# Kernel tuning notes

Measured on AMD Instinct MI355X. Metric: run time of the kernel, lower is better.

Reference implementation:

```python
import jax, jax.numpy as jnp
import numpy as np

TOP_K = 2


def setup_inputs() -> dict:
    key = jax.random.key(0)
    k0, k1, k2, k3 = jax.random.split(key, 4)
    B, S, H, I, E = 4, 2048, 1024, 2048, 8
    x = jax.random.normal(k0, (B, S, H), dtype=jnp.float32)
    Wr = jax.random.normal(k1, (H, E), dtype=jnp.float32) * 0.02
    W1 = jax.random.normal(k2, (E, H, 2 * I), dtype=jnp.float32) * 0.02
    W2 = jax.random.normal(k3, (E, I, H), dtype=jnp.float32) * 0.02
    return {"x": x, "Wr": Wr, "W1": W1, "W2": W2}


def reference(x, Wr, W1, W2):
    B, S, H = x.shape
    E = W1.shape[0]
    I = W2.shape[1]
    xf = x.reshape(-1, H)  # [T, H], T = B*S

    # Top-k router
    logits = xf @ Wr                              # [T, E]
    probs = jax.nn.softmax(logits, axis=-1)
    rw, sel = jax.lax.top_k(probs, TOP_K)          # [T, k], [T, k]
    rw = rw.astype(jnp.float32)
    rw = rw / rw.sum(axis=-1, keepdims=True)

    out = jnp.zeros_like(xf)
    for e in range(E):
        # combined gate weight for this expert per token (0 if not routed here)
        g = (rw * (sel == e)).sum(axis=-1)         # [T]
        h = xf @ W1[e]                             # [T, 2I]
        gate, up = h[:, :I], h[:, I:]
        eo = (jax.nn.silu(gate) * up) @ W2[e]      # [T, H]
        out = out + g[:, None] * eo
    return out.reshape(B, S, H)
```

## Files before the change

### kernel.cpp

```cpp
#include <hip/hip_runtime.h>
#include <hip/hip_bf16.h>

#define NTOK   8192
#define HDIM   1024
#define NEXP   8
#define IDIM   2048
#define TOTAL  (NTOK*2)

typedef short bf16x8 __attribute__((ext_vector_type(8)));
typedef float f32x4  __attribute__((ext_vector_type(4)));

__device__ __forceinline__ unsigned short f2bf(float f) {
  __hip_bfloat16 h = __float2bfloat16(f);
  return *reinterpret_cast<unsigned short*>(&h);
}
__device__ __forceinline__ float bf2f(unsigned short u) {
  __hip_bfloat16 h = *reinterpret_cast<__hip_bfloat16*>(&u);
  return __bfloat162float(h);
}

__device__ __forceinline__ void lds_load16(const unsigned short* gsrc, unsigned short* lds_base_uniform) {
  __builtin_amdgcn_global_load_lds(
      (const __attribute__((address_space(1))) unsigned int*)gsrc,
      (__attribute__((address_space(3))) unsigned int*)lds_base_uniform,
      16, 0, 0);
}

__global__ void router_kernel(const float* __restrict__ x, const float* __restrict__ Wr,
                              int* __restrict__ sel, float* __restrict__ selw,
                              int* __restrict__ counts) {
  int t = blockIdx.x * 4 + (threadIdx.x >> 6);
  int lane = threadIdx.x & 63;
  float acc[NEXP];
#pragma unroll
  for (int e = 0; e < NEXP; ++e) acc[e] = 0.f;
  const float* xr = x + (size_t)t * HDIM;
  for (int h = lane; h < HDIM; h += 64) {
    float xv = xr[h];
    const float* wr = Wr + h * NEXP;
#pragma unroll
    for (int e = 0; e < NEXP; ++e) acc[e] += xv * wr[e];
  }
#pragma unroll
  for (int off = 32; off > 0; off >>= 1) {
#pragma unroll
    for (int e = 0; e < NEXP; ++e) acc[e] += __shfl_xor(acc[e], off, 64);
  }
  if (lane == 0) {
    int i0 = 0; float v0 = acc[0];
#pragma unroll
    for (int e = 1; e < NEXP; ++e) if (acc[e] > v0) { v0 = acc[e]; i0 = e; }
    int i1 = -1; float v1 = -1e30f;
#pragma unroll
    for (int e = 0; e < NEXP; ++e) if (e != i0 && acc[e] > v1) { v1 = acc[e]; i1 = e; }
    float e1 = expf(v1 - v0);
    float w0 = 1.f / (1.f + e1);
    float w1 = e1 / (1.f + e1);
    sel[t*2] = i0; sel[t*2+1] = i1;
    selw[t*2] = w0; selw[t*2+1] = w1;
    atomicAdd(&counts[i0], 1);
    atomicAdd(&counts[i1], 1);
  }
}

__global__ void prefix_kernel(const int* __restrict__ counts, int* __restrict__ offsets,
                              int* __restrict__ cursor) {
  if (threadIdx.x == 0) {
    int s = 0;
    for (int e = 0; e < NEXP; ++e) { offsets[e] = s; cursor[e] = s; s += counts[e]; }
    offsets[NEXP] = s;
  }
}

__global__ void scatter_kernel(const int* __restrict__ sel, const float* __restrict__ selw,
                               int* __restrict__ cursor, int* __restrict__ token_ids,
                               float* __restrict__ gates) {
  int t = blockIdx.x * 256 + threadIdx.x;
  if (t >= NTOK) return;
#pragma unroll
  for (int k = 0; k < 2; ++k) {
    int e = sel[t*2+k];
    int p = atomicAdd(&cursor[e], 1);
    token_ids[p] = t;
    gates[p] = selw[t*2+k];
  }
}

__global__ void xsplit_kernel(const float* __restrict__ x, unsigned short* __restrict__ Xs) {
  int t = blockIdx.x;
  const float4* src = reinterpret_cast<const float4*>(x + (size_t)t * HDIM);
  float4 v = src[threadIdx.x];
  unsigned short h0 = f2bf(v.x), h1 = f2bf(v.y), h2 = f2bf(v.z), h3 = f2bf(v.w);
  ushort4 hi = { h0, h1, h2, h3 };
  ushort4 lo = { f2bf(v.x - bf2f(h0)), f2bf(v.y - bf2f(h1)),
                 f2bf(v.z - bf2f(h2)), f2bf(v.w - bf2f(h3)) };
  *reinterpret_cast<ushort4*>(Xs + (size_t)t*2*HDIM + threadIdx.x*4) = hi;
  *reinterpret_cast<ushort4*>(Xs + (size_t)t*2*HDIM + HDIM + threadIdx.x*4) = lo;
}

__global__ void split_transpose_kernel(const float* __restrict__ W, unsigned short* __restrict__ WT,
                                       int R, int C) {
  int e = blockIdx.z;
  int c0 = blockIdx.x * 64, r0 = blockIdx.y * 64;
  __shared__ unsigned short hiT[64][65];
  __shared__ unsigned short loT[64][65];
  int tx = threadIdx.x & 63, ty = threadIdx.x >> 6;
  const float* src = W + ((size_t)e * R + r0) * C + c0;
#pragma unroll
  for (int rr = 0; rr < 16; ++rr) {
    int r_l = ty * 16 + rr;
    float v = src[(size_t)r_l * C + tx];
    unsigned short h = f2bf(v);
    hiT[tx][r_l] = h;
    loT[tx][r_l] = f2bf(v - bf2f(h));
  }
  __syncthreads();
  unsigned short* dst = WT + ((size_t)e * C + c0) * (size_t)(2*R) + r0;
#pragma unroll
  for (int ww = 0; ww < 16; ++ww) {
    int c_l = ty * 16 + ww;
    dst[(size_t)c_l * (2*R) + tx]     = hiT[c_l][tx];
    dst[(size_t)c_l * (2*R) + R + tx] = loT[c_l][tx];
  }
}

__global__ __launch_bounds__(256)
void gemm1_kernel(const unsigned short* __restrict__ Xs,
                  const unsigned short* __restrict__ W1sT,
                  unsigned short* __restrict__ actS,
                  const int* __restrict__ offsets,
                  const int* __restrict__ token_ids) {
  int e = blockIdx.z;
  int off = offsets[e];
  int cnt = offsets[e+1] - off;
  int r0 = blockIdx.x * 128;
  if (r0 >= cnt) return;
  int j0 = blockIdx.y * 64;

  __shared__ unsigned short As[128*32];
  __shared__ unsigned short Bg[64*32];
  __shared__ unsigned short Bu[64*32];

  int tid = threadIdx.x;
  int lane = tid & 63, wv = tid >> 6;
  int l15 = lane & 15, lq = lane >> 4;

  f32x4 accg[2][4], accu[2][4];
#pragma unroll
  for (int m = 0; m < 2; ++m)
#pragma unroll
    for (int n = 0; n < 4; ++n) {
      accg[m][n] = f32x4{0.f, 0.f, 0.f, 0.f};
      accu[m][n] = f32x4{0.f, 0.f, 0.f, 0.f};
    }

  const unsigned short* w1e = W1sT + (size_t)e * 4096 * 2048;

  int oa0 = wv*1024 + lane*16;
  int oa1 = 4096 + oa0;
  int rowA0 = oa0 >> 6, cbA0 = (oa0 & 63) >> 1;
  int rowA1 = oa1 >> 6, cbA1 = (oa1 & 63) >> 1;
  int gpA0 = off + r0 + rowA0; if (gpA0 > TOTAL-1) gpA0 = TOTAL-1;
  int gpA1 = off + r0 + rowA1; if (gpA1 > TOTAL-1) gpA1 = TOTAL-1;
  int tA0 = token_ids[gpA0];
  int tA1 = token_ids[gpA1];
  const unsigned short* srcA0 = Xs + (size_t)tA0*2048 + cbA0;
  const unsigned short* srcA1 = Xs + (size_t)tA1*2048 + cbA1;
  int ob = wv*1024 + lane*16;
  int colB = ob >> 6, kbB = (ob & 63) >> 1;

  for (int ks = 0; ks < 96; ++ks) {
    int s  = ks >> 5;
    int k0 = (ks & 31) << 5;
    int acol = ((s == 1) ? HDIM : 0) + k0;
    int bk   = ((s == 2) ? HDIM : 0) + k0;

    lds_load16(srcA0 + acol, (unsigned short*)((char*)As + wv*1024));
    lds_load16(srcA1 + acol, (unsigned short*)((char*)As + 4096 + wv*1024));
    lds_load16(w1e + (size_t)(j0 + colB)*2048 + bk + kbB,        (unsigned short*)((char*)Bg + wv*1024));
    lds_load16(w1e + (size_t)(IDIM + j0 + colB)*2048 + bk + kbB, (unsigned short*)((char*)Bu + wv*1024));
    __syncthreads();

    bf16x8 af[2], bgf[4], buf2[4];
#pragma unroll
    for (int m = 0; m < 2; ++m)
      af[m] = *reinterpret_cast<const bf16x8*>(&As[(wv*32 + m*16 + l15)*32 + lq*8]);
#pragma unroll
    for (int n = 0; n < 4; ++n) {
      bgf[n]  = *reinterpret_cast<const bf16x8*>(&Bg[(n*16 + l15)*32 + lq*8]);
      buf2[n] = *reinterpret_cast<const bf16x8*>(&Bu[(n*16 + l15)*32 + lq*8]);
    }
#pragma unroll
    for (int m = 0; m < 2; ++m)
#pragma unroll
      for (int n = 0; n < 4; ++n) {
        accg[m][n] = __builtin_amdgcn_mfma_f32_16x16x32_bf16(af[m], bgf[n], accg[m][n], 0, 0, 0);
        accu[m][n] = __builtin_amdgcn_mfma_f32_16x16x32_bf16(af[m], buf2[n], accu[m][n], 0, 0, 0);
      }
    __syncthreads();
  }

#pragma unroll
  for (int m = 0; m < 2; ++m) {
#pragma unroll
    for (int rr = 0; rr < 4; ++rr) {
      int lrow = r0 + wv*32 + m*16 + lq*4 + rr;
      if (lrow < cnt) {
        size_t prow = (size_t)(off + lrow);
#pragma unroll
        for (int n = 0; n < 4; ++n) {
          float g = accg[m][n][rr], u = accu[m][n][rr];
          float a = (g / (1.f + expf(-g))) * u;
          unsigned short hh = f2bf(a);
          unsigned short ll = f2bf(a - bf2f(hh));
          int col = j0 + n*16 + l15;
          actS[prow*4096 + col]        = hh;
          actS[prow*4096 + IDIM + col] = ll;
        }
      }
    }
  }
}

__global__ __launch_bounds__(256)
void gemm2_kernel(const unsigned short* __restrict__ actS,
                  const unsigned short* __restrict__ W2sT,
                  const int* __restrict__ offsets,
                  const int* __restrict__ token_ids,
                  const float* __restrict__ gates,
                  float* __restrict__ out) {
  int e = blockIdx.z;
  int off = offsets[e];
  int cnt = offsets[e+1] - off;
  int r0 = blockIdx.x * 128;
  if (r0 >= cnt) return;
  int c0 = blockIdx.y * 128;

  __shared__ unsigned short As[128*32];
  __shared__ unsigned short Bs[128*32];

  int tid = threadIdx.x;
  int lane = tid & 63, wv = tid >> 6;
  int l15 = lane & 15, lq = lane >> 4;

  f32x4 acc[2][8];
#pragma unroll
  for (int m = 0; m < 2; ++m)
#pragma unroll
    for (int n = 0; n < 8; ++n) acc[m][n] = f32x4{0.f, 0.f, 0.f, 0.f};

  const unsigned short* w2e = W2sT + (size_t)e * 1024 * 4096;

  int oa0 = wv*1024 + lane*16;
  int oa1 = 4096 + oa0;
  int rowA0 = oa0 >> 6, cbA0 = (oa0 & 63) >> 1;
  int rowA1 = oa1 >> 6, cbA1 = (oa1 & 63) >> 1;
  int gpA0 = off + r0 + rowA0; if (gpA0 > TOTAL-1) gpA0 = TOTAL-1;
  int gpA1 = off + r0 + rowA1; if (gpA1 > TOTAL-1) gpA1 = TOTAL-1;
  int colB0 = oa0 >> 6, kbB0 = (oa0 & 63) >> 1;
  int colB1 = oa1 >> 6, kbB1 = (oa1 & 63) >> 1;

  for (int ks = 0; ks < 192; ++ks) {
    int s  = ks >> 6;
    int k0 = (ks & 63) << 5;
    int acol = ((s == 1) ? IDIM : 0) + k0;
    int bk   = ((s == 2) ? IDIM : 0) + k0;

    lds_load16(actS + (size_t)gpA0*4096 + acol + cbA0, (unsigned short*)((char*)As + wv*1024));
    lds_load16(actS + (size_t)gpA1*4096 + acol + cbA1, (unsigned short*)((char*)As + 4096 + wv*1024));
    lds_load16(w2e + (size_t)(c0 + colB0)*4096 + bk + kbB0, (unsigned short*)((char*)Bs + wv*1024));
    lds_load16(w2e + (size_t)(c0 + colB1)*4096 + bk + kbB1, (unsigned short*)((char*)Bs + 4096 + wv*1024));
    __syncthreads();

    bf16x8 af[2], bfr[8];
#pragma unroll
    for (int m = 0; m < 2; ++m)
      af[m] = *reinterpret_cast<const bf16x8*>(&As[(wv*32 + m*16 + l15)*32 + lq*8]);
#pragma unroll
    for (int n = 0; n < 8; ++n)
      bfr[n] = *reinterpret_cast<const bf16x8*>(&Bs[(n*16 + l15)*32 + lq*8]);
#pragma unroll
    for (int m = 0; m < 2; ++m)
#pragma unroll
      for (int n = 0; n < 8; ++n)
        acc[m][n] = __builtin_amdgcn_mfma_f32_16x16x32_bf16(af[m], bfr[n], acc[m][n], 0, 0, 0);
    __syncthreads();
  }

#pragma unroll
  for (int m = 0; m < 2; ++m) {
#pragma unroll
    for (int rr = 0; rr < 4; ++rr) {
      int lrow = r0 + wv*32 + m*16 + lq*4 + rr;
      if (lrow < cnt) {
        int pos = off + lrow;
        int t = token_ids[pos];
        float w = gates[pos];
        float* orow = out + (size_t)t * HDIM;
#pragma unroll
        for (int n = 0; n < 8; ++n)
          atomicAdd(&orow[c0 + n*16 + l15], w * acc[m][n][rr]);
      }
    }
  }
}

extern "C" void kernel_launch(void* const* d_in, const int* in_sizes, int n_in,
                              void* d_out, int out_size, void* d_ws, size_t ws_size,
                              hipStream_t stream) {
  (void)in_sizes; (void)n_in;
  const float* x  = (const float*)d_in[0];
  const float* Wr = (const float*)d_in[1];
  const float* W1 = (const float*)d_in[2];
  const float* W2 = (const float*)d_in[3];
  float* out = (float*)d_out;

  char* ws = (char*)d_ws;
  int*   counts    = (int*)(ws + 0);
  int*   offsets   = (int*)(ws + 64);
  int*   cursor    = (int*)(ws + 128);
  int*   sel       = (int*)(ws + 4096);
  float* selw      = (float*)(ws + 4096 + 65536);
  int*   token_ids = (int*)(ws + 4096 + 2*65536);
  float* gates     = (float*)(ws + 4096 + 3*65536);
  const size_t XS_OFF   = 266240ULL;
  const size_t W1T_OFF  = XS_OFF  + 33554432ULL;
  const size_t W2T_OFF  = W1T_OFF + 134217728ULL;
  const size_t ACT_OFF  = W2T_OFF + 67108864ULL;
  const size_t REQUIRED = ACT_OFF + 134217728ULL;
  unsigned short* Xs   = (unsigned short*)(ws + XS_OFF);
  unsigned short* W1sT = (unsigned short*)(ws + W1T_OFF);
  unsigned short* W2sT = (unsigned short*)(ws + W2T_OFF);
  unsigned short* actS = (unsigned short*)(ws + ACT_OFF);

  hipMemsetAsync(d_out, 0, (size_t)out_size * sizeof(float), stream);
  if (ws_size < REQUIRED) return;

  hipMemsetAsync(counts, 0, 64, stream);
  router_kernel<<<NTOK/4, 256, 0, stream>>>(x, Wr, sel, selw, counts);
  prefix_kernel<<<1, 64, 0, stream>>>(counts, offsets, cursor);
  scatter_kernel<<<NTOK/256, 256, 0, stream>>>(sel, selw, cursor, token_ids, gates);
  xsplit_kernel<<<NTOK, 256, 0, stream>>>(x, Xs);
  split_transpose_kernel<<<dim3(64, 16, NEXP), 256, 0, stream>>>(W1, W1sT, 1024, 4096);
  split_transpose_kernel<<<dim3(16, 32, NEXP), 256, 0, stream>>>(W2, W2sT, 2048, 1024);
  gemm1_kernel<<<dim3(64, 32, NEXP), 256, 0, stream>>>(Xs, W1sT, actS, offsets, token_ids);
  gemm2_kernel<<<dim3(64, 8, NEXP), 256, 0, stream>>>(actS, W2sT, offsets, token_ids, gates, out);
}
```

Before: 1.986 ms.

## Double K tile to 64 with XOR-swizzled LDS layout in both MoE GEMMs

```diff
diff --git a/kernel.cpp b/kernel.cpp
--- a/kernel.cpp
+++ b/kernel.cpp
@@ -137,13 +137,39 @@
   if (r0 >= cnt) return;
   int j0 = blockIdx.y * 64;
 
-  __shared__ unsigned short As[128*32];
-  __shared__ unsigned short Bg[64*32];
-  __shared__ unsigned short Bu[64*32];
+  __shared__ unsigned short As[128*64];
+  __shared__ unsigned short Bg[64*64];
+  __shared__ unsigned short Bu[64*64];
 
   int tid = threadIdx.x;
   int lane = tid & 63, wv = tid >> 6;
   int l15 = lane & 15, lq = lane >> 4;
+  int lr = lane >> 3;
+  int g  = lane & 7;
+
+  const unsigned short* w1e = W1sT + (size_t)e * 4096 * 2048;
+
+  const unsigned short* srcA[4]; unsigned short* dstA[4];
+#pragma unroll
+  for (int i = 0; i < 4; ++i) {
+    int rowt = wv*32 + i*8 + lr;
+    int gp = off + r0 + rowt; if (gp > TOTAL-1) gp = TOTAL-1;
+    int tok = token_ids[gp];
+    int sg = g ^ (rowt & 7);
+    srcA[i] = Xs + (size_t)tok*2048 + sg*8;
+    dstA[i] = As + wv*2048 + i*512;
+  }
+  const unsigned short* srcBg[2]; const unsigned short* srcBu[2];
+  unsigned short* dstBg[2]; unsigned short* dstBu[2];
+#pragma unroll
+  for (int i = 0; i < 2; ++i) {
+    int rowt = wv*16 + i*8 + lr;
+    int sg = g ^ (rowt & 7);
+    srcBg[i] = w1e + (size_t)(j0 + rowt)*2048 + sg*8;
+    srcBu[i] = w1e + (size_t)(IDIM + j0 + rowt)*2048 + sg*8;
+    dstBg[i] = Bg + wv*1024 + i*512;
+    dstBu[i] = Bu + wv*1024 + i*512;
+  }
 
   f32x4 accg[2][4], accu[2][4];
 #pragma unroll
@@ -154,49 +180,41 @@
       accu[m][n] = f32x4{0.f, 0.f, 0.f, 0.f};
     }
 
-  const unsigned short* w1e = W1sT + (size_t)e * 4096 * 2048;
-
-  int oa0 = wv*1024 + lane*16;
-  int oa1 = 4096 + oa0;
-  int rowA0 = oa0 >> 6, cbA0 = (oa0 & 63) >> 1;
-  int rowA1 = oa1 >> 6, cbA1 = (oa1 & 63) >> 1;
-  int gpA0 = off + r0 + rowA0; if (gpA0 > TOTAL-1) gpA0 = TOTAL-1;
-  int gpA1 = off + r0 + rowA1; if (gpA1 > TOTAL-1) gpA1 = TOTAL-1;
-  int tA0 = token_ids[gpA0];
-  int tA1 = token_ids[gpA1];
-  const unsigned short* srcA0 = Xs + (size_t)tA0*2048 + cbA0;
-  const unsigned short* srcA1 = Xs + (size_t)tA1*2048 + cbA1;
-  int ob = wv*1024 + lane*16;
-  int colB = ob >> 6, kbB = (ob & 63) >> 1;
-
-  for (int ks = 0; ks < 96; ++ks) {
-    int s  = ks >> 5;
-    int k0 = (ks & 31) << 5;
-    int acol = ((s == 1) ? HDIM : 0) + k0;
-    int bk   = ((s == 2) ? HDIM : 0) + k0;
-
-    lds_load16(srcA0 + acol, (unsigned short*)((char*)As + wv*1024));
-    lds_load16(srcA1 + acol, (unsigned short*)((char*)As + 4096 + wv*1024));
-    lds_load16(w1e + (size_t)(j0 + colB)*2048 + bk + kbB,        (unsigned short*)((char*)Bg + wv*1024));
-    lds_load16(w1e + (size_t)(IDIM + j0 + colB)*2048 + bk + kbB, (unsigned short*)((char*)Bu + wv*1024));
+  for (int ks = 0; ks < 48; ++ks) {
+    int s  = ks >> 4;
+    int k0 = (ks & 15) << 6;
+    int aoff = ((s == 1) ? HDIM : 0) + k0;
+    int boff = ((s == 2) ? HDIM : 0) + k0;
+
+#pragma unroll
+    for (int i = 0; i < 4; ++i) lds_load16(srcA[i] + aoff, dstA[i]);
+#pragma unroll
+    for (int i = 0; i < 2; ++i) {
+      lds_load16(srcBg[i] + boff, dstBg[i]);
+      lds_load16(srcBu[i] + boff, dstBu[i]);
+    }
     __syncthreads();
 
-    bf16x8 af[2], bgf[4], buf2[4];
-#pragma unroll
-    for (int m = 0; m < 2; ++m)
-      af[m] = *reinterpret_cast<const bf16x8*>(&As[(wv*32 + m*16 + l15)*32 + lq*8]);
-#pragma unroll
-    for (int n = 0; n < 4; ++n) {
-      bgf[n]  = *reinterpret_cast<const bf16x8*>(&Bg[(n*16 + l15)*32 + lq*8]);
-      buf2[n] = *reinterpret_cast<const bf16x8*>(&Bu[(n*16 + l15)*32 + lq*8]);
-    }
-#pragma unroll
-    for (int m = 0; m < 2; ++m)
+#pragma unroll
+    for (int kk = 0; kk < 2; ++kk) {
+      int gg = ((kk*4 + lq) ^ (l15 & 7)) * 8;
+      bf16x8 af[2], bgf[4], buf2[4];
+#pragma unroll
+      for (int m = 0; m < 2; ++m)
+        af[m] = *reinterpret_cast<const bf16x8*>(&As[(wv*32 + m*16 + l15)*64 + gg]);
 #pragma unroll
       for (int n = 0; n < 4; ++n) {
-        accg[m][n] = __builtin_amdgcn_mfma_f32_16x16x32_bf16(af[m], bgf[n], accg[m][n], 0, 0, 0);
-        accu[m][n] = __builtin_amdgcn_mfma_f32_16x16x32_bf16(af[m], buf2[n], accu[m][n], 0, 0, 0);
+        bgf[n]  = *reinterpret_cast<const bf16x8*>(&Bg[(n*16 + l15)*64 + gg]);
+        buf2[n] = *reinterpret_cast<const bf16x8*>(&Bu[(n*16 + l15)*64 + gg]);
       }
+#pragma unroll
+      for (int m = 0; m < 2; ++m)
+#pragma unroll
+        for (int n = 0; n < 4; ++n) {
+          accg[m][n] = __builtin_amdgcn_mfma_f32_16x16x32_bf16(af[m], bgf[n], accg[m][n], 0, 0, 0);
+          accu[m][n] = __builtin_amdgcn_mfma_f32_16x16x32_bf16(af[m], buf2[n], accu[m][n], 0, 0, 0);
+        }
+    }
     __syncthreads();
   }
 
@@ -209,8 +227,8 @@
         size_t prow = (size_t)(off + lrow);
 #pragma unroll
         for (int n = 0; n < 4; ++n) {
-          float g = accg[m][n][rr], u = accu[m][n][rr];
-          float a = (g / (1.f + expf(-g))) * u;
+          float gte = accg[m][n][rr], u = accu[m][n][rr];
+          float a = (gte / (1.f + expf(-gte))) * u;
           unsigned short hh = f2bf(a);
           unsigned short ll = f2bf(a - bf2f(hh));
           int col = j0 + n*16 + l15;
@@ -236,12 +254,29 @@
   if (r0 >= cnt) return;
   int c0 = blockIdx.y * 128;
 
-  __shared__ unsigned short As[128*32];
-  __shared__ unsigned short Bs[128*32];
+  __shared__ unsigned short As[128*64];
+  __shared__ unsigned short Bs[128*64];
 
   int tid = threadIdx.x;
   int lane = tid & 63, wv = tid >> 6;
   int l15 = lane & 15, lq = lane >> 4;
+  int lr = lane >> 3;
+  int g  = lane & 7;
+
+  const unsigned short* w2e = W2sT + (size_t)e * 1024 * 4096;
+
+  const unsigned short* srcA[4]; unsigned short* dstA[4];
+  const unsigned short* srcB[4]; unsigned short* dstB[4];
+#pragma unroll
+  for (int i = 0; i < 4; ++i) {
+    int rowt = wv*32 + i*8 + lr;
+    int gp = off + r0 + rowt; if (gp > TOTAL-1) gp = TOTAL-1;
+    int sg = g ^ (rowt & 7);
+    srcA[i] = actS + (size_t)gp*4096 + sg*8;
+    dstA[i] = As + wv*2048 + i*512;
+    srcB[i] = w2e + (size_t)(c0 + rowt)*4096 + sg*8;
+    dstB[i] = Bs + wv*2048 + i*512;
+  }
 
   f32x4 acc[2][8];
 #pragma unroll
@@ -249,41 +284,35 @@
 #pragma unroll
     for (int n = 0; n < 8; ++n) acc[m][n] = f32x4{0.f, 0.f, 0.f, 0.f};
 
-  const unsigned short* w2e = W2sT + (size_t)e * 1024 * 4096;
-
-  int oa0 = wv*1024 + lane*16;
-  int oa1 = 4096 + oa0;
-  int rowA0 = oa0 >> 6, cbA0 = (oa0 & 63) >> 1;
-  int rowA1 = oa1 >> 6, cbA1 = (oa1 & 63) >> 1;
-  int gpA0 = off + r0 + rowA0; if (gpA0 > TOTAL-1) gpA0 = TOTAL-1;
-  int gpA1 = off + r0 + rowA1; if (gpA1 > TOTAL-1) gpA1 = TOTAL-1;
-  int colB0 = oa0 >> 6, kbB0 = (oa0 & 63) >> 1;
-  int colB1 = oa1 >> 6, kbB1 = (oa1 & 63) >> 1;
-
-  for (int ks = 0; ks < 192; ++ks) {
-    int s  = ks >> 6;
-    int k0 = (ks & 63) << 5;
-    int acol = ((s == 1) ? IDIM : 0) + k0;
-    int bk   = ((s == 2) ? IDIM : 0) + k0;
-
-    lds_load16(actS + (size_t)gpA0*4096 + acol + cbA0, (unsigned short*)((char*)As + wv*1024));
-    lds_load16(actS + (size_t)gpA1*4096 + acol + cbA1, (unsigned short*)((char*)As + 4096 + wv*1024));
-    lds_load16(w2e + (size_t)(c0 + colB0)*4096 + bk + kbB0, (unsigned short*)((char*)Bs + wv*1024));
-    lds_load16(w2e + (size_t)(c0 + colB1)*4096 + bk + kbB1, (unsigned short*)((char*)Bs + 4096 + wv*1024));
+  for (int ks = 0; ks < 96; ++ks) {
+    int s  = ks >> 5;
+    int k0 = (ks & 31) << 6;
+    int aoff = ((s == 1) ? IDIM : 0) + k0;
+    int boff = ((s == 2) ? IDIM : 0) + k0;
+
+#pragma unroll
+    for (int i = 0; i < 4; ++i) {
+      lds_load16(srcA[i] + aoff, dstA[i]);
+      lds_load16(srcB[i] + boff, dstB[i]);
+    }
     __syncthreads();
 
-    bf16x8 af[2], bfr[8];
-#pragma unroll
-    for (int m = 0; m < 2; ++m)
-      af[m] = *reinterpret_cast<const bf16x8*>(&As[(wv*32 + m*16 + l15)*32 + lq*8]);
-#pragma unroll
-    for (int n = 0; n < 8; ++n)
-      bfr[n] = *reinterpret_cast<const bf16x8*>(&Bs[(n*16 + l15)*32 + lq*8]);
-#pragma unroll
-    for (int m = 0; m < 2; ++m)
+#pragma unroll
+    for (int kk = 0; kk < 2; ++kk) {
+      int gg = ((kk*4 + lq) ^ (l15 & 7)) * 8;
+      bf16x8 af[2], bfr[8];
+#pragma unroll
+      for (int m = 0; m < 2; ++m)
+        af[m] = *reinterpret_cast<const bf16x8*>(&As[(wv*32 + m*16 + l15)*64 + gg]);
 #pragma unroll
       for (int n = 0; n < 8; ++n)
-        acc[m][n] = __builtin_amdgcn_mfma_f32_16x16x32_bf16(af[m], bfr[n], acc[m][n], 0, 0, 0);
+        bfr[n] = *reinterpret_cast<const bf16x8*>(&Bs[(n*16 + l15)*64 + gg]);
+#pragma unroll
+      for (int m = 0; m < 2; ++m)
+#pragma unroll
+        for (int n = 0; n < 8; ++n)
+          acc[m][n] = __builtin_amdgcn_mfma_f32_16x16x32_bf16(af[m], bfr[n], acc[m][n], 0, 0, 0);
+    }
     __syncthreads();
   }
 
```

After: 1.836 ms. 7.6% less time.
